# Kernel optimization log

Measured on AMD Instinct MI355X. Metric: run time of the kernel, lower is better.

Reference implementation:

```python
import jax, jax.numpy as jnp
import numpy as np

B, C, P, GH, GW = 32, 3, 32, 8, 16
DIM, DEPTH, HEADS, DHEAD = 1024, 12, 16, 64
N = GH * GW              # 128 tokens
PATCH_DIM = C * P * P    # 3072
INNER = HEADS * DHEAD    # 1024
EPS = 1e-5


def layer_norm(x, g, b):
    mu = jnp.mean(x, axis=-1, keepdims=True)
    var = jnp.var(x, axis=-1, keepdims=True)
    return (x - mu) * jax.lax.rsqrt(var + EPS) * g + b


def setup_inputs() -> dict:
    key = jax.random.key(0)
    ks = iter(jax.random.split(key, 32))
    s = 0.02
    inp = {
        "img": jax.random.normal(next(ks), (B, C, GH * P, GW * P), jnp.float32),
        "sph_pos": jax.random.uniform(next(ks), (GH, GW, 2), jnp.float32),
        "sph_dist": jax.random.uniform(next(ks), (N, N), jnp.float32),
        # patch embedding conv (kernel == stride == patch)
        "conv_w": jax.random.normal(next(ks), (DIM, C, P, P), jnp.float32) * s,
        "conv_b": jnp.zeros((DIM,), jnp.float32),
        # norm_linear: LN -> Linear(dim,dim) -> LN
        "nl_ln1_g": jnp.ones((DIM,), jnp.float32),
        "nl_ln1_b": jnp.zeros((DIM,), jnp.float32),
        "nl_w": jax.random.normal(next(ks), (DIM, DIM), jnp.float32) * s,
        "nl_b": jnp.zeros((DIM,), jnp.float32),
        "nl_ln2_g": jnp.ones((DIM,), jnp.float32),
        "nl_ln2_b": jnp.zeros((DIM,), jnp.float32),
        # pos embedding Linear(2, dim)
        "pos_w": jax.random.normal(next(ks), (2, DIM), jnp.float32) * s,
        "pos_b": jnp.zeros((DIM,), jnp.float32),
        # per-layer attention params, stacked over depth
        "ln_g": jnp.ones((DEPTH, DIM), jnp.float32),
        "ln_b": jnp.zeros((DEPTH, DIM), jnp.float32),
        "wqkv": jax.random.normal(next(ks), (DEPTH, DIM, 3 * INNER), jnp.float32) * s,
        "wo": jax.random.normal(next(ks), (DEPTH, INNER, DIM), jnp.float32) * s,
        "wo_b": jnp.zeros((DEPTH, DIM), jnp.float32),
        # final transformer LN
        "tr_ln_g": jnp.ones((DIM,), jnp.float32),
        "tr_ln_b": jnp.zeros((DIM,), jnp.float32),
        # expand head: Linear(dim, patch_dim) + LN(patch_dim)
        "exp_w": jax.random.normal(next(ks), (DIM, PATCH_DIM), jnp.float32) * s,
        "exp_b": jnp.zeros((PATCH_DIM,), jnp.float32),
        "out_ln_g": jnp.ones((PATCH_DIM,), jnp.float32),
        "out_ln_b": jnp.zeros((PATCH_DIM,), jnp.float32),
    }
    return inp


def _forward(img, sph_pos, sph_dist, conv_w, conv_b, nl_ln1_g, nl_ln1_b, nl_w,
             nl_b, nl_ln2_g, nl_ln2_b, pos_w, pos_b, ln_g, ln_b, wqkv, wo,
             wo_b, tr_ln_g, tr_ln_b, exp_w, exp_b, out_ln_g, out_ln_b):
    b = img.shape[0]
    scale = DHEAD ** -0.5
    # patch embedding: Conv2d(kernel=stride=P) == per-patch linear
    patches = img.reshape(b, C, GH, P, GW, P)  # b c h p w q
    x = jnp.einsum('bchpwq,dcpq->bhwd', patches, conv_w) + conv_b  # [b,GH,GW,dim]
    x = x.reshape(b, N, DIM)
    # norm_linear
    x = layer_norm(x, nl_ln1_g, nl_ln1_b)
    x = x @ nl_w + nl_b
    x = layer_norm(x, nl_ln2_g, nl_ln2_b)
    # spherical positional embedding
    pos = (sph_pos @ pos_w + pos_b).reshape(N, DIM)
    x = x + pos[None]
    # transformer: GlobalSphereAttention blocks with residuals
    bias = 1.0 + sph_dist  # [N,N]
    for l in range(DEPTH):
        h = layer_norm(x, ln_g[l], ln_b[l])
        qkv = h @ wqkv[l]  # [b,n,3*inner]
        q, k, v = jnp.split(qkv, 3, axis=-1)
        q = q.reshape(b, N, HEADS, DHEAD).transpose(0, 2, 1, 3)
        k = k.reshape(b, N, HEADS, DHEAD).transpose(0, 2, 1, 3)
        v = v.reshape(b, N, HEADS, DHEAD).transpose(0, 2, 1, 3)
        dots = jnp.einsum('bhid,bhjd->bhij', q, k) * scale
        w = dots * bias  # broadcast over b,h
        # cross-head standardization (torch.std -> ddof=1)
        mu = jnp.mean(w, axis=1, keepdims=True)
        sd = jnp.std(w, axis=1, keepdims=True, ddof=1)
        attn = jax.nn.softmax((w - mu) / sd, axis=-1)
        o = jnp.einsum('bhij,bhjd->bhid', attn, v)
        o = o.transpose(0, 2, 1, 3).reshape(b, N, INNER)
        x = o @ wo[l] + wo_b[l] + x
    x = layer_norm(x, tr_ln_g, tr_ln_b)
    # expand and reassemble image: 'b (h w) (p1 p2 c) -> b c (h p1) (w p2)'
    x = layer_norm(x @ exp_w + exp_b, out_ln_g, out_ln_b)  # [b,N,patch_dim]
    x = x.reshape(b, GH, GW, P, P, C)
    x = x.transpose(0, 5, 1, 3, 2, 4).reshape(b, C, GH * P, GW * P)
    return x


def reference(img, sph_pos, sph_dist, conv_w, conv_b, nl_ln1_g, nl_ln1_b, nl_w,
              nl_b, nl_ln2_g, nl_ln2_b, pos_w, pos_b, ln_g, ln_b, wqkv, wo,
              wo_b, tr_ln_g, tr_ln_b, exp_w, exp_b, out_ln_g, out_ln_b):
    return _forward(img, sph_pos, sph_dist, conv_w, conv_b, nl_ln1_g, nl_ln1_b,
                    nl_w, nl_b, nl_ln2_g, nl_ln2_b, pos_w, pos_b, ln_g, ln_b,
                    wqkv, wo, wo_b, tr_ln_g, tr_ln_b, exp_w, exp_b, out_ln_g,
                    out_ln_b)
```

## Files before the change

kernel.cpp:

```cpp
#include <hip/hip_runtime.h>
#include <stdint.h>


typedef __attribute__((ext_vector_type(8))) short short8;
typedef __attribute__((ext_vector_type(4))) float f32x4;

#define EPS 1e-5f

__device__ __forceinline__ float b2f(ushort u) {
    union { uint32_t i; float f; } c; c.i = ((uint32_t)u) << 16; return c.f;
}
__device__ __forceinline__ ushort f2b(float f) {
    union { float f; uint32_t i; } c; c.f = f;
    uint32_t u = c.i;
    uint32_t r = (u + 0x7fffu + ((u >> 16) & 1u)) >> 16;
    return (ushort)r;
}
__device__ __forceinline__ float pack2(ushort lo, ushort hi) {
    union { uint32_t u; float f; } c;
    c.u = (uint32_t)lo | ((uint32_t)hi << 16);
    return c.f;
}
__device__ __forceinline__ short8 as_short8(f32x4 v) {
    union { f32x4 f; short8 s; } u; u.f = v; return u.s;
}
__device__ __forceinline__ void async16(const ushort* g, ushort* l) {
    __builtin_amdgcn_global_load_lds(
        (const __attribute__((address_space(1))) uint32_t*)g,
        (__attribute__((address_space(3))) uint32_t*)l, 16, 0, 0);
}

__device__ __forceinline__ float2 block_sum2(float s, float ss, int tid) {
    #pragma unroll
    for (int o = 32; o; o >>= 1) { s += __shfl_xor(s, o); ss += __shfl_xor(ss, o); }
    __shared__ float ps[4], pss[4];
    int w = tid >> 6;
    if ((tid & 63) == 0) { ps[w] = s; pss[w] = ss; }
    __syncthreads();
    return make_float2(ps[0] + ps[1] + ps[2] + ps[3],
                       pss[0] + pss[1] + pss[2] + pss[3]);
}

__global__ void sniff_dtype(const uint32_t* __restrict__ ones, int* __restrict__ flag) {
    if (threadIdx.x == 0 && blockIdx.x == 0) {
        int c32 = 0, c16 = 0;
        for (int i = 0; i < 256; i++) {
            uint32_t w = ones[i];
            c32 += (w == 0x3F800000u);
            c16 += (w == 0x3F803F80u);
        }
        *flag = (c32 >= c16) ? 1 : 0;
    }
}

template <int MODE>
__global__ __launch_bounds__(256) void gemm_nt(
    const ushort* __restrict__ A, const ushort* __restrict__ Bt,
    const void* __restrict__ bias, int bias_off, const int* __restrict__ flagp,
    float* __restrict__ Cf, ushort* __restrict__ Cb,
    int M, int N, int K, int ldA, int ldB, int ldC, int RM, int RN)
{
    __shared__ ushort As[128 * 32];
    __shared__ ushort Bs[128 * 32];
    const int tid = threadIdx.x, lane = tid & 63, w = tid >> 6;

    int lid = blockIdx.y * gridDim.x + blockIdx.x;
    int xcd = lid & 7, slot = lid >> 3;
    int regions_n = gridDim.x / RN;
    int r_m = xcd / regions_n, r_n = xcd % regions_n;
    int tm = r_m * RM + slot / RN;
    int tn = r_n * RN + slot % RN;
    const int m0 = tm * 128, n0 = tn * 128;

    const int wr = (w >> 1) * 64, wc = (w & 1) * 64;
    const int m16 = lane & 15, quad = lane >> 4;

    f32x4 acc[4][4];
    #pragma unroll
    for (int i = 0; i < 4; i++)
        #pragma unroll
        for (int j = 0; j < 4; j++) acc[i][j] = (f32x4){0.f, 0.f, 0.f, 0.f};

    const int idx0 = (w * 2) * 64 + lane, idx1 = (w * 2 + 1) * 64 + lane;
    const int row0 = idx0 >> 2, ks0 = (idx0 & 3) * 8;
    const int row1 = idx1 >> 2, ks1 = (idx1 & 3) * 8;
    const ushort* a0 = A  + (size_t)(m0 + row0) * ldA + ks0;
    const ushort* a1 = A  + (size_t)(m0 + row1) * ldA + ks1;
    const ushort* b0 = Bt + (size_t)(n0 + row0) * ldB + ks0;
    const ushort* b1 = Bt + (size_t)(n0 + row1) * ldB + ks1;

    for (int k0 = 0; k0 < K; k0 += 32) {
        __syncthreads();
        async16(a0 + k0, As + (w * 2 + 0) * 512);
        async16(a1 + k0, As + (w * 2 + 1) * 512);
        async16(b0 + k0, Bs + (w * 2 + 0) * 512);
        async16(b1 + k0, Bs + (w * 2 + 1) * 512);
        __syncthreads();
        short8 a[4], b[4];
        #pragma unroll
        for (int t = 0; t < 4; t++)
            a[t] = *(const short8*)(As + (wr + t * 16 + m16) * 32 + quad * 8);
        #pragma unroll
        for (int t = 0; t < 4; t++)
            b[t] = *(const short8*)(Bs + (wc + t * 16 + m16) * 32 + quad * 8);
        #pragma unroll
        for (int i = 0; i < 4; i++)
            #pragma unroll
            for (int j = 0; j < 4; j++)
                acc[i][j] = __builtin_amdgcn_mfma_f32_16x16x32_bf16(a[i], b[j], acc[i][j], 0, 0, 0);
    }

    float bvals[4] = {0.f, 0.f, 0.f, 0.f};
    if (bias) {
        if (*flagp) {
            #pragma unroll
            for (int j = 0; j < 4; j++)
                bvals[j] = ((const float*)bias)[bias_off + n0 + wc + j * 16 + m16];
        } else {
            #pragma unroll
            for (int j = 0; j < 4; j++)
                bvals[j] = b2f(((const ushort*)bias)[bias_off + n0 + wc + j * 16 + m16]);
        }
    }
    #pragma unroll
    for (int i = 0; i < 4; i++)
        #pragma unroll
        for (int j = 0; j < 4; j++)
            #pragma unroll
            for (int r = 0; r < 4; r++) {
                int row = m0 + wr + i * 16 + quad * 4 + r;
                int col = n0 + wc + j * 16 + m16;
                float v = acc[i][j][r] + bvals[j];
                if (MODE == 0)      Cf[(size_t)row * ldC + col] = v;
                else if (MODE == 1) Cb[(size_t)row * ldC + col] = f2b(v);
                else                Cf[(size_t)row * ldC + col] += v;
            }
}

__global__ __launch_bounds__(256) void transpose_k(
    const void* __restrict__ W, size_t eoff, ushort* __restrict__ Wt,
    int K, int N, const int* __restrict__ flagp)
{
    __shared__ ushort t[32][33];
    int f32 = *flagp;
    int n0 = blockIdx.x * 32, k0 = blockIdx.y * 32;
    int tx = threadIdx.x & 31, ty = threadIdx.x >> 5;
    if (f32) {
        const float* Wf = (const float*)W + eoff;
        #pragma unroll
        for (int i = ty; i < 32; i += 8) t[i][tx] = f2b(Wf[(size_t)(k0 + i) * N + n0 + tx]);
    } else {
        const ushort* Wb = (const ushort*)W + eoff;
        #pragma unroll
        for (int i = ty; i < 32; i += 8) t[i][tx] = Wb[(size_t)(k0 + i) * N + n0 + tx];
    }
    __syncthreads();
    #pragma unroll
    for (int i = ty; i < 32; i += 8) Wt[(size_t)(n0 + i) * K + k0 + tx] = t[tx][i];
}

__global__ __launch_bounds__(256) void convert_copy(
    const void* __restrict__ src, ushort* __restrict__ dst,
    const int* __restrict__ flagp)
{
    size_t i = ((size_t)blockIdx.x * 256 + threadIdx.x) * 8;
    if (*flagp) {
        const float* s = (const float*)src + i;
        ushort t[8];
        #pragma unroll
        for (int x = 0; x < 8; x++) t[x] = f2b(s[x]);
        *(uint4*)(dst + i) = *(uint4*)t;
    } else {
        *(uint4*)(dst + i) = *(const uint4*)((const ushort*)src + i);
    }
}

__global__ __launch_bounds__(256) void patch_gather(
    const void* __restrict__ img, ushort* __restrict__ Ap,
    const int* __restrict__ flagp)
{
    int t = blockIdx.x * 256 + threadIdx.x;
    int qc = t & 3;
    int p  = (t >> 2) & 31;
    int c  = (t >> 7) % 3;
    int rest = t / 384;
    int wg = rest & 15;
    int hg = (rest >> 4) & 7;
    int b  = rest >> 7;
    size_t si = ((size_t)((b * 3 + c) * 256 + hg * 32 + p)) * 512 + wg * 32 + qc * 8;
    size_t di = ((size_t)((b * 8 + hg) * 16 + wg)) * 3072 + c * 1024 + p * 32 + qc * 8;
    if (*flagp) {
        const float* s = (const float*)img + si;
        ushort tmp[8];
        #pragma unroll
        for (int x = 0; x < 8; x++) tmp[x] = f2b(s[x]);
        *(uint4*)(Ap + di) = *(uint4*)tmp;
    } else {
        *(uint4*)(Ap + di) = *(const uint4*)((const ushort*)img + si);
    }
}

__global__ __launch_bounds__(256) void ln_f32_to_bf16(
    const float* __restrict__ X, const void* __restrict__ g,
    const void* __restrict__ b, int goff, const int* __restrict__ flagp,
    ushort* __restrict__ Y)
{
    int row = blockIdx.x, tid = threadIdx.x;
    float4 v = ((const float4*)(X + (size_t)row * 1024))[tid];
    float s = v.x + v.y + v.z + v.w;
    float ss = v.x * v.x + v.y * v.y + v.z * v.z + v.w * v.w;
    float2 r = block_sum2(s, ss, tid);
    float mu = r.x * (1.f / 1024.f);
    float var = fmaxf(r.y * (1.f / 1024.f) - mu * mu, 0.f);
    float rs = rsqrtf(var + EPS);
    int c0 = tid * 4;
    float gv[4], bv[4];
    if (*flagp) {
        #pragma unroll
        for (int x = 0; x < 4; x++) { gv[x] = ((const float*)g)[goff + c0 + x]; bv[x] = ((const float*)b)[goff + c0 + x]; }
    } else {
        #pragma unroll
        for (int x = 0; x < 4; x++) { gv[x] = b2f(((const ushort*)g)[goff + c0 + x]); bv[x] = b2f(((const ushort*)b)[goff + c0 + x]); }
    }
    ushort4 o4;
    o4.x = f2b((v.x - mu) * rs * gv[0] + bv[0]);
    o4.y = f2b((v.y - mu) * rs * gv[1] + bv[1]);
    o4.z = f2b((v.z - mu) * rs * gv[2] + bv[2]);
    o4.w = f2b((v.w - mu) * rs * gv[3] + bv[3]);
    *(ushort4*)(Y + (size_t)row * 1024 + c0) = o4;
}

__global__ __launch_bounds__(256) void ln2_pos(
    float* __restrict__ X, const void* __restrict__ g, const void* __restrict__ b,
    const void* __restrict__ sph_pos, const void* __restrict__ pos_w,
    const void* __restrict__ pos_b, const int* __restrict__ flagp)
{
    int f32 = *flagp;
    int row = blockIdx.x, tid = threadIdx.x;
    float4 v = ((const float4*)(X + (size_t)row * 1024))[tid];
    float s = v.x + v.y + v.z + v.w;
    float ss = v.x * v.x + v.y * v.y + v.z * v.z + v.w * v.w;
    float2 r = block_sum2(s, ss, tid);
    float mu = r.x * (1.f / 1024.f);
    float var = fmaxf(r.y * (1.f / 1024.f) - mu * mu, 0.f);
    float rs = rsqrtf(var + EPS);
    int n = row & 127;
    int c0 = tid * 4;
    float s0, s1, gv[4], bv[4], w0[4], w1[4], pb[4];
    if (f32) {
        s0 = ((const float*)sph_pos)[n * 2 + 0]; s1 = ((const float*)sph_pos)[n * 2 + 1];
        #pragma unroll
        for (int x = 0; x < 4; x++) {
            gv[x] = ((const float*)g)[c0 + x];  bv[x] = ((const float*)b)[c0 + x];
            w0[x] = ((const float*)pos_w)[c0 + x]; w1[x] = ((const float*)pos_w)[1024 + c0 + x];
            pb[x] = ((const float*)pos_b)[c0 + x];
        }
    } else {
        s0 = b2f(((const ushort*)sph_pos)[n * 2 + 0]); s1 = b2f(((const ushort*)sph_pos)[n * 2 + 1]);
        #pragma unroll
        for (int x = 0; x < 4; x++) {
            gv[x] = b2f(((const ushort*)g)[c0 + x]);  bv[x] = b2f(((const ushort*)b)[c0 + x]);
            w0[x] = b2f(((const ushort*)pos_w)[c0 + x]); w1[x] = b2f(((const ushort*)pos_w)[1024 + c0 + x]);
            pb[x] = b2f(((const ushort*)pos_b)[c0 + x]);
        }
    }
    float4 o;
    o.x = (v.x - mu) * rs * gv[0] + bv[0] + s0 * w0[0] + s1 * w1[0] + pb[0];
    o.y = (v.y - mu) * rs * gv[1] + bv[1] + s0 * w0[1] + s1 * w1[1] + pb[1];
    o.z = (v.z - mu) * rs * gv[2] + bv[2] + s0 * w0[2] + s1 * w1[2] + pb[2];
    o.w = (v.w - mu) * rs * gv[3] + bv[3] + s0 * w0[3] + s1 * w1[3] + pb[3];
    *(float4*)(X + (size_t)row * 1024 + c0) = o;
}

__global__ __launch_bounds__(256) void attn_fused(
    const ushort* __restrict__ qkv, const void* __restrict__ sph_dist,
    const int* __restrict__ flagp, ushort* __restrict__ o)
{
    __shared__ float dotsf[16 * 16 * 128];
    __shared__ float musd[16 * 128 * 2];
    const int tid = threadIdx.x, lane = tid & 63, w = tid >> 6;
    const int m16 = lane & 15, quad = lane >> 4;
    const int b = blockIdx.x & 31, i0 = (blockIdx.x >> 5) * 16;
    const int f32 = *flagp;

    float sphm[8][4];
    #pragma unroll
    for (int ct = 0; ct < 8; ct++)
        #pragma unroll
        for (int r = 0; r < 4; r++) {
            int i = i0 + quad * 4 + r, j = ct * 16 + m16;
            float sd = f32 ? ((const float*)sph_dist)[i * 128 + j]
                           : b2f(((const ushort*)sph_dist)[i * 128 + j]);
            sphm[ct][r] = 0.125f * (1.f + sd);
        }

    const ushort* qrow = qkv + (size_t)(b * 128 + i0 + m16) * 3072 + quad * 8;
    const ushort* krow = qkv + (size_t)(b * 128 + m16) * 3072 + 1024 + quad * 8;
    #pragma unroll
    for (int hh = 0; hh < 4; hh++) {
        const int h = w * 4 + hh;
        short8 qa0 = *(const short8*)(qrow + h * 64);
        short8 qa1 = *(const short8*)(qrow + h * 64 + 32);
        f32x4 acc[8];
        #pragma unroll
        for (int ct = 0; ct < 8; ct++) acc[ct] = (f32x4){0.f, 0.f, 0.f, 0.f};
        #pragma unroll
        for (int ct = 0; ct < 8; ct++) {
            const ushort* kp = krow + (size_t)ct * 16 * 3072 + h * 64;
            short8 k0 = *(const short8*)(kp);
            short8 k1 = *(const short8*)(kp + 32);
            acc[ct] = __builtin_amdgcn_mfma_f32_16x16x32_bf16(qa0, k0, acc[ct], 0, 0, 0);
            acc[ct] = __builtin_amdgcn_mfma_f32_16x16x32_bf16(qa1, k1, acc[ct], 0, 0, 0);
        }
        #pragma unroll
        for (int ct = 0; ct < 8; ct++)
            #pragma unroll
            for (int r = 0; r < 4; r++)
                dotsf[h * 2048 + (quad * 4 + r) * 128 + ct * 16 + m16] =
                    acc[ct][r] * sphm[ct][r];
    }
    __syncthreads();

    #pragma unroll
    for (int p = 0; p < 8; p++) {
        int idx = p * 256 + tid, i = idx >> 7, j = idx & 127;
        float v[16], s = 0.f;
        #pragma unroll
        for (int h = 0; h < 16; h++) { v[h] = dotsf[h * 2048 + i * 128 + j]; s += v[h]; }
        float mu = s * (1.f / 16.f), q = 0.f;
        #pragma unroll
        for (int h = 0; h < 16; h++) { float d = v[h] - mu; q += d * d; }
        float rsd = rsqrtf(fmaxf(q * (1.f / 15.f), 1e-20f));
        musd[(i * 128 + j) * 2]     = mu;
        musd[(i * 128 + j) * 2 + 1] = rsd;
    }
    __syncthreads();

    #pragma unroll
    for (int hh = 0; hh < 4; hh++) {
        const int h = w * 4 + hh;
        #pragma unroll
        for (int i = 0; i < 16; i++) {
            float x0 = dotsf[h * 2048 + i * 128 + 2 * lane];
            float x1 = dotsf[h * 2048 + i * 128 + 2 * lane + 1];
            float4 ms = *(const float4*)&musd[i * 256 + 4 * lane];
            x0 = (x0 - ms.x) * ms.y;
            x1 = (x1 - ms.z) * ms.w;
            float m = fmaxf(x0, x1);
            #pragma unroll
            for (int o2 = 32; o2; o2 >>= 1) m = fmaxf(m, __shfl_xor(m, o2));
            float e0 = __expf(x0 - m), e1 = __expf(x1 - m);
            float s = e0 + e1;
            #pragma unroll
            for (int o2 = 32; o2; o2 >>= 1) s += __shfl_xor(s, o2);
            float inv = 1.f / s;
            dotsf[h * 2048 + i * 64 + (lane ^ ((i & 7) << 2))] =
                pack2(f2b(e0 * inv), f2b(e1 * inv));
        }
    }
    __syncthreads();

    #pragma unroll 1
    for (int g = 0; g < 4; g++) {
        const int h = w * 4 + g;
        {
            const ushort* vr0 = qkv + (size_t)(b * 128 + 2 * lane) * 3072 + 2048 + h * 64;
            const ushort* vr1 = vr0 + 3072;
            short8 r0[8], r1[8];
            #pragma unroll
            for (int x = 0; x < 8; x++) {
                r0[x] = *(const short8*)(vr0 + x * 8);
                r1[x] = *(const short8*)(vr1 + x * 8);
            }
            #pragma unroll
            for (int d = 0; d < 64; d++)
                dotsf[(w * 4 + (d >> 4)) * 2048 + 1024 + (d & 15) * 64 +
                      (lane ^ ((d & 7) << 2))] =
                    pack2((ushort)r0[d >> 3][d & 7], (ushort)r1[d >> 3][d & 7]);
        }
        __syncthreads();
        f32x4 pacc[4];
        #pragma unroll
        for (int ct = 0; ct < 4; ct++) pacc[ct] = (f32x4){0.f, 0.f, 0.f, 0.f};
        const int sw = (m16 & 7) << 2;
        #pragma unroll
        for (int kq = 0; kq < 4; kq++) {
            f32x4 paw = *(const f32x4*)&dotsf[h * 2048 + m16 * 64 +
                                              ((kq * 16 + quad * 4) ^ sw)];
            short8 pa = as_short8(paw);
            #pragma unroll
            for (int ct = 0; ct < 4; ct++) {
                f32x4 vbw = *(const f32x4*)&dotsf[(w * 4 + ct) * 2048 + 1024 + m16 * 64 +
                                                  ((kq * 16 + quad * 4) ^ sw)];
                pacc[ct] = __builtin_amdgcn_mfma_f32_16x16x32_bf16(pa, as_short8(vbw), pacc[ct], 0, 0, 0);
            }
        }
        #pragma unroll
        for (int ct = 0; ct < 4; ct++)
            #pragma unroll
            for (int r = 0; r < 4; r++)
                o[(size_t)(b * 128 + i0 + quad * 4 + r) * 1024 + h * 64 + ct * 16 + m16] =
                    f2b(pacc[ct][r]);
        __syncthreads();
    }
}

__global__ __launch_bounds__(256) void out_ln_rearrange(
    const ushort* __restrict__ Y, const void* __restrict__ g,
    const void* __restrict__ bb, const int* __restrict__ flagp,
    void* __restrict__ out)
{
    __shared__ float rowbuf[3072];
    int f32 = *flagp;
    int r = blockIdx.x;
    int b = r >> 7, n = r & 127, hg = n >> 4, wg = n & 15;
    int tid = threadIdx.x;
    float s = 0.f, ss = 0.f;
    #pragma unroll
    for (int x = 0; x < 3; x++) {
        ushort4 u = *(const ushort4*)(Y + (size_t)r * 3072 + (size_t)(x * 256 + tid) * 4);
        float4 v = make_float4(b2f(u.x), b2f(u.y), b2f(u.z), b2f(u.w));
        *(float4*)(rowbuf + (x * 256 + tid) * 4) = v;
        s += v.x + v.y + v.z + v.w;
        ss += v.x * v.x + v.y * v.y + v.z * v.z + v.w * v.w;
    }
    float2 red = block_sum2(s, ss, tid);
    float mu = red.x * (1.f / 3072.f);
    float var = fmaxf(red.y * (1.f / 3072.f) - mu * mu, 0.f);
    float rs = rsqrtf(var + EPS);
    int p1 = tid >> 3, sj = tid & 7;
    #pragma unroll
    for (int c = 0; c < 3; c++) {
        float vals[4];
        #pragma unroll
        for (int x = 0; x < 4; x++) {
            int p2 = sj * 4 + x;
            int col = p1 * 96 + p2 * 3 + c;
            float gv, bv;
            if (f32) { gv = ((const float*)g)[col];  bv = ((const float*)bb)[col]; }
            else     { gv = b2f(((const ushort*)g)[col]); bv = b2f(((const ushort*)bb)[col]); }
            vals[x] = (rowbuf[col] - mu) * rs * gv + bv;
        }
        size_t di = (size_t)((b * 3 + c) * 256 + hg * 32 + p1) * 512 + wg * 32 + sj * 4;
        if (f32) {
            *(float4*)((float*)out + di) = make_float4(vals[0], vals[1], vals[2], vals[3]);
        } else {
            ushort4 o4;
            #pragma unroll
            for (int x = 0; x < 4; x++) ((ushort*)&o4)[x] = f2b(vals[x]);
            *(ushort4*)((ushort*)out + di) = o4;
        }
    }
}

extern "C" void kernel_launch(void* const* d_in, const int* in_sizes, int n_in,
                              void* d_out, int out_size, void* d_ws, size_t ws_size,
                              hipStream_t stream)
{
    const void* img      = d_in[0];
    const void* sph_pos  = d_in[1];
    const void* sph_dist = d_in[2];
    const void* conv_w   = d_in[3];
    const void* conv_b   = d_in[4];
    const void* nl1g     = d_in[5];
    const void* nl1b     = d_in[6];
    const void* nl_w     = d_in[7];
    const void* nl_b     = d_in[8];
    const void* nl2g     = d_in[9];
    const void* nl2b     = d_in[10];
    const void* pos_w    = d_in[11];
    const void* pos_b    = d_in[12];
    const void* ln_g     = d_in[13];
    const void* ln_b     = d_in[14];
    const void* wqkv     = d_in[15];
    const void* wo       = d_in[16];
    const void* wo_b     = d_in[17];
    const void* trg      = d_in[18];
    const void* trb      = d_in[19];
    const void* exp_w    = d_in[20];
    const void* exp_b    = d_in[21];
    const void* og       = d_in[22];
    const void* ob       = d_in[23];

    char* ws = (char*)d_ws;
    float*  xf    = (float*) (ws + 0);
    ushort* xb    = (ushort*)(ws + 16777216);
    ushort* qkvb  = (ushort*)(ws + 25165824);
    float*  y1    = (float*) (ws + 50331648);
    ushort* o_bf  = (ushort*)(ws + 50331648);
    ushort* wTa   = (ushort*)(ws + 83886080);
    ushort* wTb   = (ushort*)(ws + 90177536);
    int*    flagp = (int*)   (ws + 92274688);

    sniff_dtype<<<1, 64, 0, stream>>>((const uint32_t*)nl1g, flagp);

    patch_gather<<<6144, 256, 0, stream>>>(img, qkvb, flagp);
    convert_copy<<<1536, 256, 0, stream>>>(conv_w, wTa, flagp);
    gemm_nt<0><<<dim3(8, 32), 256, 0, stream>>>(qkvb, wTa, conv_b, 0, flagp, y1, nullptr,
                                                4096, 1024, 3072, 3072, 3072, 1024, 4, 8);
    ln_f32_to_bf16<<<4096, 256, 0, stream>>>(y1, nl1g, nl1b, 0, flagp, xb);
    transpose_k<<<dim3(32, 32), 256, 0, stream>>>(nl_w, 0, wTb, 1024, 1024, flagp);
    gemm_nt<0><<<dim3(8, 32), 256, 0, stream>>>(xb, wTb, nl_b, 0, flagp, xf, nullptr,
                                                4096, 1024, 1024, 1024, 1024, 1024, 4, 8);
    ln2_pos<<<4096, 256, 0, stream>>>(xf, nl2g, nl2b, sph_pos, pos_w, pos_b, flagp);

    for (int l = 0; l < 12; l++) {
        transpose_k<<<dim3(96, 32), 256, 0, stream>>>(wqkv, (size_t)l * 1024 * 3072, wTa, 1024, 3072, flagp);
        transpose_k<<<dim3(32, 32), 256, 0, stream>>>(wo, (size_t)l * 1024 * 1024, wTb, 1024, 1024, flagp);
        ln_f32_to_bf16<<<4096, 256, 0, stream>>>(xf, ln_g, ln_b, l * 1024, flagp, xb);
        gemm_nt<1><<<dim3(24, 32), 256, 0, stream>>>(xb, wTa, nullptr, 0, flagp, nullptr, qkvb,
                                                     4096, 3072, 1024, 1024, 1024, 3072, 8, 12);
        attn_fused<<<256, 256, 0, stream>>>(qkvb, sph_dist, flagp, o_bf);
        gemm_nt<2><<<dim3(8, 32), 256, 0, stream>>>(o_bf, wTb, wo_b, l * 1024, flagp, xf, nullptr,
                                                    4096, 1024, 1024, 1024, 1024, 1024, 4, 8);
    }

    ln_f32_to_bf16<<<4096, 256, 0, stream>>>(xf, trg, trb, 0, flagp, xb);
    transpose_k<<<dim3(96, 32), 256, 0, stream>>>(exp_w, 0, wTa, 1024, 3072, flagp);
    gemm_nt<1><<<dim3(24, 32), 256, 0, stream>>>(xb, wTa, exp_b, 0, flagp, nullptr, qkvb,
                                                 4096, 3072, 1024, 1024, 1024, 3072, 8, 12);
    out_ln_rearrange<<<4096, 256, 0, stream>>>(qkvb, og, ob, flagp, d_out);
}
```

Baseline: 2.179 ms.

## Triple-buffer GEMM LDS tiles with async prefetch two K-steps ahead

Replaces the single-buffered K loop of the bf16 MFMA GEMM with a three-stage ring of shared-memory tiles. Global-to-LDS async loads for step t+2 are issued before computing step t, and explicit vmcnt waits plus barriers control when each stage is consumed. This hides global memory latency behind MFMA work instead of stalling at every K step. The cost is three times the LDS footprint per block (about 48 KB), which may lower occupancy, and the correctness now depends on hand-written waitcnt values.

```diff
diff --git a/kernel.cpp b/kernel.cpp
--- a/kernel.cpp
+++ b/kernel.cpp
@@ -60,8 +60,8 @@
     float* __restrict__ Cf, ushort* __restrict__ Cb,
     int M, int N, int K, int ldA, int ldB, int ldC, int RM, int RN)
 {
-    __shared__ ushort As[128 * 32];
-    __shared__ ushort Bs[128 * 32];
+    __shared__ ushort As[3 * 128 * 32];
+    __shared__ ushort Bs[3 * 128 * 32];
     const int tid = threadIdx.x, lane = tid & 63, w = tid >> 6;
 
     int lid = blockIdx.y * gridDim.x + blockIdx.x;
@@ -89,25 +89,57 @@
     const ushort* b0 = Bt + (size_t)(n0 + row0) * ldB + ks0;
     const ushort* b1 = Bt + (size_t)(n0 + row1) * ldB + ks1;
 
-    for (int k0 = 0; k0 < K; k0 += 32) {
-        __syncthreads();
-        async16(a0 + k0, As + (w * 2 + 0) * 512);
-        async16(a1 + k0, As + (w * 2 + 1) * 512);
-        async16(b0 + k0, Bs + (w * 2 + 0) * 512);
-        async16(b1 + k0, Bs + (w * 2 + 1) * 512);
-        __syncthreads();
+    const int nt = K >> 5;
+    const int c0 = (w * 2 + 0) * 512;
+    const int c1 = (w * 2 + 1) * 512;
+
+    async16(a0, As + c0);
+    async16(a1, As + c1);
+    async16(b0, Bs + c0);
+    async16(b1, Bs + c1);
+    if (nt > 1) {
+        async16(a0 + 32, As + 4096 + c0);
+        async16(a1 + 32, As + 4096 + c1);
+        async16(b0 + 32, Bs + 4096 + c0);
+        async16(b1 + 32, Bs + 4096 + c1);
+    }
+
+    int cur = 0;
+    for (int t = 0; t < nt; ++t) {
+        int b2 = cur + 2; if (b2 >= 3) b2 -= 3;
+        if (t + 2 < nt) {
+            const int ko = (t + 2) * 32;
+            async16(a0 + ko, As + b2 * 4096 + c0);
+            async16(a1 + ko, As + b2 * 4096 + c1);
+            async16(b0 + ko, Bs + b2 * 4096 + c0);
+            async16(b1 + ko, Bs + b2 * 4096 + c1);
+            asm volatile("s_waitcnt vmcnt(8)" ::: "memory");
+        } else if (t + 1 < nt) {
+            asm volatile("s_waitcnt vmcnt(4)" ::: "memory");
+        } else {
+            asm volatile("s_waitcnt vmcnt(0)" ::: "memory");
+        }
+        __builtin_amdgcn_s_barrier();
+        __builtin_amdgcn_sched_barrier(0);
+
+        const ushort* Ac = As + cur * 4096;
+        const ushort* Bc = Bs + cur * 4096;
         short8 a[4], b[4];
         #pragma unroll
-        for (int t = 0; t < 4; t++)
-            a[t] = *(const short8*)(As + (wr + t * 16 + m16) * 32 + quad * 8);
-        #pragma unroll
-        for (int t = 0; t < 4; t++)
-            b[t] = *(const short8*)(Bs + (wc + t * 16 + m16) * 32 + quad * 8);
+        for (int t4 = 0; t4 < 4; t4++)
+            a[t4] = *(const short8*)(Ac + (wr + t4 * 16 + m16) * 32 + quad * 8);
+        #pragma unroll
+        for (int t4 = 0; t4 < 4; t4++)
+            b[t4] = *(const short8*)(Bc + (wc + t4 * 16 + m16) * 32 + quad * 8);
         #pragma unroll
         for (int i = 0; i < 4; i++)
             #pragma unroll
             for (int j = 0; j < 4; j++)
                 acc[i][j] = __builtin_amdgcn_mfma_f32_16x16x32_bf16(a[i], b[j], acc[i][j], 0, 0, 0);
+
+        __builtin_amdgcn_sched_barrier(0);
+        __builtin_amdgcn_s_barrier();
+        cur = (cur + 1 == 3) ? 0 : cur + 1;
     }
 
     float bvals[4] = {0.f, 0.f, 0.f, 0.f};
```

Result: faster. 2.113 ms (-3.1%).
